# Kernel tuning notes

Measured on AMD Instinct MI355X. Metric: run time of the kernel, lower is better.

## Reference

```python
import jax, jax.numpy as jnp
import numpy as np
jax.config.update("jax_enable_x64", True)

B_GROWTH = 1.38
PS = np.array([1, 19349663, 83492791, 73856093], dtype=np.int64)
N_POINTS = 131072

def _isprime(n):
    if n < 2:
        return False
    i = 2
    while i * i <= n:
        if n % i == 0:
            return False
        i += 1
    return True

def _build_tables():
    n_levels, n_entrys, base_res, f = 16, 2 ** 19, 16, 2
    while not _isprime(n_entrys):
        n_entrys += 1
    xyz_min = np.array([-1.0, -1.0, -1.0])
    xyz_max = np.array([1.0, 1.0, 1.0])
    start_frame, end_frame, total_frame = 0, 99, 100
    bounds = np.stack([
        np.concatenate([xyz_min, [start_frame / total_frame]]),
        np.concatenate([xyz_max, [end_frame / total_frame]]),
    ]).astype(np.float32)
    sizes, nums = [], []
    for i in range(n_levels):
        grid_num = int((base_res * B_GROWTH ** i) ** 3)
        grid_size = ((xyz_max - xyz_min).prod() / grid_num) ** (1.0 / 3.0)
        world_size = (xyz_max - xyz_min) / grid_size
        nums.append(np.concatenate([world_size, [end_frame - start_frame + 1]]).astype(np.int64))
        xyz_size = (xyz_max - xyz_min) / (world_size - 1)
        sizes.append(np.concatenate([xyz_size, [1.0 / (total_frame - 1)]]))
    entrys_size = np.array(sizes, dtype=np.float32)
    entrys_num = np.array(nums, dtype=np.int64)
    start_hash = n_levels
    for i in range(n_levels):
        if int(entrys_num[i].prod()) > n_entrys:
            start_hash = i
            break
    return n_levels, n_entrys, f, bounds, entrys_size, entrys_num, start_hash, start_frame, total_frame

# 16 binary corner offsets, last coord = LSB (matches hard-coded torch table)
OFFSETS = np.array([[(i >> 3) & 1, (i >> 2) & 1, (i >> 1) & 1, i & 1] for i in range(16)], dtype=np.float32)

def setup_inputs() -> dict:
    L, T, f, bounds, entrys_size, entrys_num, start_hash, start_frame, total_frame = _build_tables()
    key = jax.random.key(0)
    k1, k2, k3 = jax.random.split(key, 3)
    xyz = jax.random.uniform(k1, (N_POINTS, 3), dtype=jnp.float32)  # inside [-1,1]^3 bbox
    t = jax.random.uniform(k2, (N_POINTS, 1), dtype=jnp.float32)
    # kaiming_normal_ on (L,T,f): fan_in = T*f, gain=sqrt(2)
    std = float(np.sqrt(2.0 / (T * f)))
    data = jax.random.normal(k3, (L, T, f), dtype=jnp.float32) * std
    return {
        "xyz": xyz, "t": t, "data": data,
        "bounds": jnp.asarray(bounds), "offsets": jnp.asarray(OFFSETS),
        "entrys_size": jnp.asarray(entrys_size), "entrys_num": jnp.asarray(entrys_num),
        "start_hash": int(start_hash), "start_frame": int(start_frame), "total_frame": int(total_frame),
    }

def reference(xyz, t, data, bounds, offsets, entrys_size, entrys_num, start_hash, start_frame, total_frame):
    L, T, f = data.shape
    N = xyz.shape[0]
    t = t - start_frame / (total_frame - 1)
    xyzt = jnp.concatenate([xyz, t], axis=-1)                                   # [N,4]
    float_xyzt = (xyzt[None] - bounds[0][None, None]) / entrys_size[:, None, :]  # [L,N,4]
    int_xyzt = (float_xyzt[:, :, None] + offsets[None, None]).astype(jnp.int64)  # [L,N,16,4]
    offset_xyzt = float_xyzt - int_xyzt[:, :, 0]                                 # [L,N,4]
    int_xyzt = jnp.clip(int_xyzt, 0, (entrys_num - 1)[:, None, None, :])
    en = entrys_num  # int64 [L,4]
    ind_direct = ((int_xyzt[..., 0] * en[:, None, None, 1] + int_xyzt[..., 1]) * en[:, None, None, 2]
                  + int_xyzt[..., 2]) * en[:, None, None, 3] + int_xyzt[..., 3]  # [L,N,16]
    ps = jnp.asarray(PS)
    ind_hash = (int_xyzt[..., 0] * ps[0] ^ int_xyzt[..., 1] * ps[1]
                ^ int_xyzt[..., 2] * ps[2] ^ int_xyzt[..., 3] * ps[3]) % T
    is_hash = (jnp.arange(L) >= start_hash)[:, None, None]
    ind = jnp.where(is_hash, ind_hash, ind_direct)                               # [L,N,16]
    val = jnp.take_along_axis(data, ind.reshape(L, -1, 1), axis=1).reshape(L, N, 16, f)
    w = jnp.clip(1.0 - offsets[None, None] + (2.0 * offsets[None, None] - 1.0) * offset_xyzt[:, :, None], 0.0, 1.0)
    w = jnp.prod(w, axis=-1)                                                     # [L,N,16]
    out = (w[..., None] * val).sum(axis=-2)                                      # [L,N,f]
    return out.transpose(1, 0, 2).reshape(N, L * f)
```

## Files before the change

kernel.cpp:

```cpp
#include <hip/hip_runtime.h>


#define FDIM 2

using f32x2 = __attribute__((ext_vector_type(2))) float;

__global__ __launch_bounds__(256) void mh4d_kernel(
    const float* __restrict__ xyz,
    const float* __restrict__ tt,
    const float* __restrict__ data,
    const float* __restrict__ bounds,
    const float* __restrict__ es,
    const int*   __restrict__ en,
    const int*   __restrict__ p_sh,
    const int*   __restrict__ p_sf,
    const int*   __restrict__ p_tf,
    float* __restrict__ out,
    int N, int L, unsigned int T, unsigned long long M,
    unsigned int bpl)
{
    int l, chunk;
    if ((L & 7) == 0) {
        const unsigned int x   = blockIdx.x & 7u;
        const unsigned int rem = blockIdx.x >> 3;
        const unsigned int p   = rem / bpl;
        chunk = (int)(rem - p * bpl);
        l     = (int)(p * 8u + x);
    } else {
        l     = (int)(blockIdx.x / bpl);
        chunk = (int)(blockIdx.x - (unsigned)l * bpl);
    }
    const int n = chunk * (int)blockDim.x + (int)threadIdx.x;
    if (n >= N) return;

    const int start_hash = *p_sh;
    const float tshift = (float)((double)(*p_sf) / (double)(*p_tf - 1));

    const float es0 = es[l * 4 + 0], es1 = es[l * 4 + 1];
    const float es2 = es[l * 4 + 2], es3 = es[l * 4 + 3];
    const int e0 = en[l * 4 + 0], e1 = en[l * 4 + 1];
    const int e2 = en[l * 4 + 2], e3 = en[l * 4 + 3];

    const float b0 = bounds[0], b1 = bounds[1], b2 = bounds[2], b3 = bounds[3];

    const float x  = __builtin_nontemporal_load(&xyz[n * 3 + 0]);
    const float y  = __builtin_nontemporal_load(&xyz[n * 3 + 1]);
    const float z  = __builtin_nontemporal_load(&xyz[n * 3 + 2]);
    const float tv = __builtin_nontemporal_load(&tt[n]) - tshift;

    const float f0 = (x  - b0) / es0;
    const float f1 = (y  - b1) / es1;
    const float f2 = (z  - b2) / es2;
    const float f3 = (tv - b3) / es3;

    int lo0 = (int)f0, hi0 = (int)(f0 + 1.0f);
    int lo1 = (int)f1, hi1 = (int)(f1 + 1.0f);
    int lo2 = (int)f2, hi2 = (int)(f2 + 1.0f);
    int lo3 = (int)f3, hi3 = (int)(f3 + 1.0f);

    const float o0 = f0 - (float)lo0;
    const float o1 = f1 - (float)lo1;
    const float o2 = f2 - (float)lo2;
    const float o3 = f3 - (float)lo3;

    lo0 = min(max(lo0, 0), e0 - 1);  hi0 = min(max(hi0, 0), e0 - 1);
    lo1 = min(max(lo1, 0), e1 - 1);  hi1 = min(max(hi1, 0), e1 - 1);
    lo2 = min(max(lo2, 0), e2 - 1);  hi2 = min(max(hi2, 0), e2 - 1);
    lo3 = min(max(lo3, 0), e3 - 1);  hi3 = min(max(hi3, 0), e3 - 1);

    unsigned int r16[16];
    if (l >= start_hash) {
        const unsigned long long hx[2] = { (unsigned long long)(unsigned)lo0,
                                           (unsigned long long)(unsigned)hi0 };
        const unsigned long long hy[2] = { (unsigned long long)(unsigned)lo1 * 19349663ull,
                                           (unsigned long long)(unsigned)hi1 * 19349663ull };
        const unsigned long long hz[2] = { (unsigned long long)(unsigned)lo2 * 83492791ull,
                                           (unsigned long long)(unsigned)hi2 * 83492791ull };
        const unsigned long long ht[2] = { (unsigned long long)(unsigned)lo3 * 73856093ull,
                                           (unsigned long long)(unsigned)hi3 * 73856093ull };
        #pragma unroll
        for (int c = 0; c < 16; ++c) {
            const unsigned long long v =
                hx[(c >> 3) & 1] ^ hy[(c >> 2) & 1] ^ hz[(c >> 1) & 1] ^ ht[c & 1];
            const unsigned long long q = __umul64hi(v, M);
            unsigned int r = (unsigned int)v - (unsigned int)q * T;
            if (r >= T) r -= T;
            r16[c] = r;
        }
    } else {
        #pragma unroll
        for (int c = 0; c < 16; ++c) {
            const unsigned int ix = (unsigned)((c & 8) ? hi0 : lo0);
            const unsigned int iy = (unsigned)((c & 4) ? hi1 : lo1);
            const unsigned int iz = (unsigned)((c & 2) ? hi2 : lo2);
            const unsigned int it = (unsigned)((c & 1) ? hi3 : lo3);
            unsigned int ind = ix * (unsigned)e1 + iy;
            ind = ind * (unsigned)e2 + iz;
            ind = ind * (unsigned)e3 + it;
            r16[c] = ind;
        }
    }

    const float* __restrict__ base = data + (size_t)l * (size_t)T * FDIM;
    f32x2 vals[16];
    #pragma unroll
    for (int c = 0; c < 16; ++c) {
        asm volatile("global_load_dwordx2 %0, %1, %2 sc0"
                     : "=v"(vals[c])
                     : "v"(r16[c] * 8u), "s"(base));
    }

    const float wx[2] = { fminf(fmaxf(1.0f - o0, 0.0f), 1.0f), fminf(fmaxf(o0, 0.0f), 1.0f) };
    const float wy[2] = { fminf(fmaxf(1.0f - o1, 0.0f), 1.0f), fminf(fmaxf(o1, 0.0f), 1.0f) };
    const float wz[2] = { fminf(fmaxf(1.0f - o2, 0.0f), 1.0f), fminf(fmaxf(o2, 0.0f), 1.0f) };
    const float wt[2] = { fminf(fmaxf(1.0f - o3, 0.0f), 1.0f), fminf(fmaxf(o3, 0.0f), 1.0f) };

    float pxy[4], pxyz[8], w16[16];
    #pragma unroll
    for (int a = 0; a < 2; ++a)
        #pragma unroll
        for (int b = 0; b < 2; ++b)
            pxy[a * 2 + b] = wx[a] * wy[b];
    #pragma unroll
    for (int a = 0; a < 4; ++a)
        #pragma unroll
        for (int b = 0; b < 2; ++b)
            pxyz[a * 2 + b] = pxy[a] * wz[b];
    #pragma unroll
    for (int a = 0; a < 8; ++a)
        #pragma unroll
        for (int b = 0; b < 2; ++b)
            w16[a * 2 + b] = pxyz[a] * wt[b];

    asm volatile("s_waitcnt vmcnt(0)" ::: "memory");
    __builtin_amdgcn_sched_barrier(0);

    float accx = 0.0f, accy = 0.0f;
    #pragma unroll
    for (int c = 0; c < 16; ++c) {
        accx = fmaf(w16[c], vals[c][0], accx);
        accy = fmaf(w16[c], vals[c][1], accy);
    }

    unsigned long long packed =
        ((unsigned long long)__float_as_uint(accy) << 32) | (unsigned long long)__float_as_uint(accx);
    unsigned long long* op =
        (unsigned long long*)(out + ((size_t)n * (size_t)L + (size_t)l) * FDIM);
    __builtin_nontemporal_store(packed, op);
}

extern "C" void kernel_launch(void* const* d_in, const int* in_sizes, int n_in,
                              void* d_out, int out_size, void* d_ws, size_t ws_size,
                              hipStream_t stream) {
    const float* xyz    = (const float*)d_in[0];
    const float* tt     = (const float*)d_in[1];
    const float* data   = (const float*)d_in[2];
    const float* bounds = (const float*)d_in[3];
    const float* es     = (const float*)d_in[5];
    const int*   en     = (const int*)d_in[6];
    const int*   p_sh   = (const int*)d_in[7];
    const int*   p_sf   = (const int*)d_in[8];
    const int*   p_tf   = (const int*)d_in[9];
    float*       out    = (float*)d_out;

    const int N = in_sizes[0] / 3;
    const int L = in_sizes[5] / 4;
    const unsigned int T = (unsigned int)(in_sizes[2] / (L * FDIM));
    const unsigned long long M = ~0ull / (unsigned long long)T;

    const int threads = 256;
    const unsigned int bpl = (unsigned)((N + threads - 1) / threads);
    dim3 grid(bpl * (unsigned)L);
    mh4d_kernel<<<grid, threads, 0, stream>>>(xyz, tt, data, bounds, es, en,
                                              p_sh, p_sf, p_tf, out,
                                              N, L, T, M, bpl);
}
```

Baseline: 261.4 us.

## Process two points per thread to overlap gathers with weight computation

Each thread now handles two points, issuing 32 gather loads up front and computing weights for the second point while the first point's loads complete. Staged waitcnt values let the first result be accumulated and stored before waiting on the second batch. The grid is halved and launch bounds request 4 blocks per CU. This trades higher register pressure and fewer waves for more memory-level parallelism per wave.

```diff
diff --git a/kernel.cpp b/kernel.cpp
--- a/kernel.cpp
+++ b/kernel.cpp
@@ -5,7 +5,7 @@
 
 using f32x2 = __attribute__((ext_vector_type(2))) float;
 
-__global__ __launch_bounds__(256) void mh4d_kernel(
+__global__ __launch_bounds__(256, 4) void mh4d_kernel(
     const float* __restrict__ xyz,
     const float* __restrict__ tt,
     const float* __restrict__ data,
@@ -21,17 +21,20 @@
 {
     int l, chunk;
     if ((L & 7) == 0) {
-        const unsigned int x   = blockIdx.x & 7u;
+        const unsigned int xb  = blockIdx.x & 7u;
         const unsigned int rem = blockIdx.x >> 3;
         const unsigned int p   = rem / bpl;
         chunk = (int)(rem - p * bpl);
-        l     = (int)(p * 8u + x);
+        l     = (int)(p * 8u + xb);
     } else {
         l     = (int)(blockIdx.x / bpl);
         chunk = (int)(blockIdx.x - (unsigned)l * bpl);
     }
-    const int n = chunk * (int)blockDim.x + (int)threadIdx.x;
-    if (n >= N) return;
+    const int nA = chunk * 2 * (int)blockDim.x + (int)threadIdx.x;
+    if (nA >= N) return;
+    const int nBr = nA + (int)blockDim.x;
+    const bool hasB = nBr < N;
+    const int nB = hasB ? nBr : nA;
 
     const int start_hash = *p_sh;
     const float tshift = (float)((double)(*p_sf) / (double)(*p_tf - 1));
@@ -43,110 +46,143 @@
 
     const float b0 = bounds[0], b1 = bounds[1], b2 = bounds[2], b3 = bounds[3];
 
-    const float x  = __builtin_nontemporal_load(&xyz[n * 3 + 0]);
-    const float y  = __builtin_nontemporal_load(&xyz[n * 3 + 1]);
-    const float z  = __builtin_nontemporal_load(&xyz[n * 3 + 2]);
-    const float tv = __builtin_nontemporal_load(&tt[n]) - tshift;
-
-    const float f0 = (x  - b0) / es0;
-    const float f1 = (y  - b1) / es1;
-    const float f2 = (z  - b2) / es2;
-    const float f3 = (tv - b3) / es3;
-
-    int lo0 = (int)f0, hi0 = (int)(f0 + 1.0f);
-    int lo1 = (int)f1, hi1 = (int)(f1 + 1.0f);
-    int lo2 = (int)f2, hi2 = (int)(f2 + 1.0f);
-    int lo3 = (int)f3, hi3 = (int)(f3 + 1.0f);
-
-    const float o0 = f0 - (float)lo0;
-    const float o1 = f1 - (float)lo1;
-    const float o2 = f2 - (float)lo2;
-    const float o3 = f3 - (float)lo3;
-
-    lo0 = min(max(lo0, 0), e0 - 1);  hi0 = min(max(hi0, 0), e0 - 1);
-    lo1 = min(max(lo1, 0), e1 - 1);  hi1 = min(max(hi1, 0), e1 - 1);
-    lo2 = min(max(lo2, 0), e2 - 1);  hi2 = min(max(hi2, 0), e2 - 1);
-    lo3 = min(max(lo3, 0), e3 - 1);  hi3 = min(max(hi3, 0), e3 - 1);
-
-    unsigned int r16[16];
-    if (l >= start_hash) {
-        const unsigned long long hx[2] = { (unsigned long long)(unsigned)lo0,
-                                           (unsigned long long)(unsigned)hi0 };
-        const unsigned long long hy[2] = { (unsigned long long)(unsigned)lo1 * 19349663ull,
-                                           (unsigned long long)(unsigned)hi1 * 19349663ull };
-        const unsigned long long hz[2] = { (unsigned long long)(unsigned)lo2 * 83492791ull,
-                                           (unsigned long long)(unsigned)hi2 * 83492791ull };
-        const unsigned long long ht[2] = { (unsigned long long)(unsigned)lo3 * 73856093ull,
-                                           (unsigned long long)(unsigned)hi3 * 73856093ull };
-        #pragma unroll
-        for (int c = 0; c < 16; ++c) {
-            const unsigned long long v =
-                hx[(c >> 3) & 1] ^ hy[(c >> 2) & 1] ^ hz[(c >> 1) & 1] ^ ht[c & 1];
-            const unsigned long long q = __umul64hi(v, M);
-            unsigned int r = (unsigned int)v - (unsigned int)q * T;
-            if (r >= T) r -= T;
-            r16[c] = r;
-        }
-    } else {
-        #pragma unroll
-        for (int c = 0; c < 16; ++c) {
-            const unsigned int ix = (unsigned)((c & 8) ? hi0 : lo0);
-            const unsigned int iy = (unsigned)((c & 4) ? hi1 : lo1);
-            const unsigned int iz = (unsigned)((c & 2) ? hi2 : lo2);
-            const unsigned int it = (unsigned)((c & 1) ? hi3 : lo3);
-            unsigned int ind = ix * (unsigned)e1 + iy;
-            ind = ind * (unsigned)e2 + iz;
-            ind = ind * (unsigned)e3 + it;
-            r16[c] = ind;
-        }
+#define LOADP(S, n) \
+    const float x##S  = __builtin_nontemporal_load(&xyz[(n) * 3 + 0]); \
+    const float y##S  = __builtin_nontemporal_load(&xyz[(n) * 3 + 1]); \
+    const float z##S  = __builtin_nontemporal_load(&xyz[(n) * 3 + 2]); \
+    const float tv##S = __builtin_nontemporal_load(&tt[(n)]) - tshift;
+
+    LOADP(A, nA)
+    LOADP(B, nB)
+
+#define CORNERS(S) \
+    const float f0##S = (x##S  - b0) / es0; \
+    const float f1##S = (y##S  - b1) / es1; \
+    const float f2##S = (z##S  - b2) / es2; \
+    const float f3##S = (tv##S - b3) / es3; \
+    int lo0##S = (int)f0##S, hi0##S = (int)(f0##S + 1.0f); \
+    int lo1##S = (int)f1##S, hi1##S = (int)(f1##S + 1.0f); \
+    int lo2##S = (int)f2##S, hi2##S = (int)(f2##S + 1.0f); \
+    int lo3##S = (int)f3##S, hi3##S = (int)(f3##S + 1.0f); \
+    const float o0##S = f0##S - (float)lo0##S; \
+    const float o1##S = f1##S - (float)lo1##S; \
+    const float o2##S = f2##S - (float)lo2##S; \
+    const float o3##S = f3##S - (float)lo3##S; \
+    lo0##S = min(max(lo0##S, 0), e0 - 1);  hi0##S = min(max(hi0##S, 0), e0 - 1); \
+    lo1##S = min(max(lo1##S, 0), e1 - 1);  hi1##S = min(max(hi1##S, 0), e1 - 1); \
+    lo2##S = min(max(lo2##S, 0), e2 - 1);  hi2##S = min(max(hi2##S, 0), e2 - 1); \
+    lo3##S = min(max(lo3##S, 0), e3 - 1);  hi3##S = min(max(hi3##S, 0), e3 - 1);
+
+    CORNERS(A)
+    CORNERS(B)
+
+#define INDICES(S, r) \
+    if (l >= start_hash) { \
+        const unsigned long long hx[2] = { (unsigned long long)(unsigned)lo0##S, \
+                                           (unsigned long long)(unsigned)hi0##S }; \
+        const unsigned long long hy[2] = { (unsigned long long)(unsigned)lo1##S * 19349663ull, \
+                                           (unsigned long long)(unsigned)hi1##S * 19349663ull }; \
+        const unsigned long long hz[2] = { (unsigned long long)(unsigned)lo2##S * 83492791ull, \
+                                           (unsigned long long)(unsigned)hi2##S * 83492791ull }; \
+        const unsigned long long ht[2] = { (unsigned long long)(unsigned)lo3##S * 73856093ull, \
+                                           (unsigned long long)(unsigned)hi3##S * 73856093ull }; \
+        _Pragma("unroll") \
+        for (int c = 0; c < 16; ++c) { \
+            const unsigned long long v = \
+                hx[(c >> 3) & 1] ^ hy[(c >> 2) & 1] ^ hz[(c >> 1) & 1] ^ ht[c & 1]; \
+            const unsigned long long q = __umul64hi(v, M);    \
+            unsigned int rr = (unsigned int)v - (unsigned int)q * T; \
+            if (rr >= T) rr -= T; \
+            (r)[c] = rr; \
+        } \
+    } else { \
+        _Pragma("unroll") \
+        for (int c = 0; c < 16; ++c) { \
+            const unsigned int ix = (unsigned)((c & 8) ? hi0##S : lo0##S); \
+            const unsigned int iy = (unsigned)((c & 4) ? hi1##S : lo1##S); \
+            const unsigned int iz = (unsigned)((c & 2) ? hi2##S : lo2##S); \
+            const unsigned int it = (unsigned)((c & 1) ? hi3##S : lo3##S); \
+            unsigned int ind = ix * (unsigned)e1 + iy; \
+            ind = ind * (unsigned)e2 + iz; \
+            ind = ind * (unsigned)e3 + it; \
+            (r)[c] = ind; \
+        } \
     }
 
     const float* __restrict__ base = data + (size_t)l * (size_t)T * FDIM;
-    f32x2 vals[16];
+
+    __builtin_amdgcn_sched_barrier(0);
+
+    unsigned int rA[16];
+    INDICES(A, rA)
+    f32x2 valsA[16];
+    #pragma unroll
+    for (int c = 0; c < 16; ++c)
+        asm volatile("global_load_dwordx2 %0, %1, %2 sc0"
+                     : "=v"(valsA[c]) : "v"(rA[c] * 8u), "s"(base));
+
+    unsigned int rB[16];
+    INDICES(B, rB)
+    f32x2 valsB[16];
+    #pragma unroll
+    for (int c = 0; c < 16; ++c)
+        asm volatile("global_load_dwordx2 %0, %1, %2 sc0"
+                     : "=v"(valsB[c]) : "v"(rB[c] * 8u), "s"(base));
+
+#define WEIGHTS(S, w) \
+    { \
+        const float wx[2] = { fminf(fmaxf(1.0f - o0##S, 0.0f), 1.0f), fminf(fmaxf(o0##S, 0.0f), 1.0f) }; \
+        const float wy[2] = { fminf(fmaxf(1.0f - o1##S, 0.0f), 1.0f), fminf(fmaxf(o1##S, 0.0f), 1.0f) }; \
+        const float wz[2] = { fminf(fmaxf(1.0f - o2##S, 0.0f), 1.0f), fminf(fmaxf(o2##S, 0.0f), 1.0f) }; \
+        const float wt[2] = { fminf(fmaxf(1.0f - o3##S, 0.0f), 1.0f), fminf(fmaxf(o3##S, 0.0f), 1.0f) }; \
+        float pxy[4], pxyz[8]; \
+        _Pragma("unroll") for (int a = 0; a < 2; ++a) \
+            _Pragma("unroll") for (int b = 0; b < 2; ++b) pxy[a * 2 + b] = wx[a] * wy[b]; \
+        _Pragma("unroll") for (int a = 0; a < 4; ++a) \
+            _Pragma("unroll") for (int b = 0; b < 2; ++b) pxyz[a * 2 + b] = pxy[a] * wz[b]; \
+        _Pragma("unroll") for (int a = 0; a < 8; ++a) \
+            _Pragma("unroll") for (int b = 0; b < 2; ++b) (w)[a * 2 + b] = pxyz[a] * wt[b]; \
+    }
+
+    float wA[16];
+    WEIGHTS(A, wA)
+
+    asm volatile("s_waitcnt vmcnt(16)" ::: "memory");
+    __builtin_amdgcn_sched_barrier(0);
+
+    float accxA = 0.0f, accyA = 0.0f;
     #pragma unroll
     for (int c = 0; c < 16; ++c) {
-        asm volatile("global_load_dwordx2 %0, %1, %2 sc0"
-                     : "=v"(vals[c])
-                     : "v"(r16[c] * 8u), "s"(base));
-    }
-
-    const float wx[2] = { fminf(fmaxf(1.0f - o0, 0.0f), 1.0f), fminf(fmaxf(o0, 0.0f), 1.0f) };
-    const float wy[2] = { fminf(fmaxf(1.0f - o1, 0.0f), 1.0f), fminf(fmaxf(o1, 0.0f), 1.0f) };
-    const float wz[2] = { fminf(fmaxf(1.0f - o2, 0.0f), 1.0f), fminf(fmaxf(o2, 0.0f), 1.0f) };
-    const float wt[2] = { fminf(fmaxf(1.0f - o3, 0.0f), 1.0f), fminf(fmaxf(o3, 0.0f), 1.0f) };
-
-    float pxy[4], pxyz[8], w16[16];
-    #pragma unroll
-    for (int a = 0; a < 2; ++a)
-        #pragma unroll
-        for (int b = 0; b < 2; ++b)
-            pxy[a * 2 + b] = wx[a] * wy[b];
-    #pragma unroll
-    for (int a = 0; a < 4; ++a)
-        #pragma unroll
-        for (int b = 0; b < 2; ++b)
-            pxyz[a * 2 + b] = pxy[a] * wz[b];
-    #pragma unroll
-    for (int a = 0; a < 8; ++a)
-        #pragma unroll
-        for (int b = 0; b < 2; ++b)
-            w16[a * 2 + b] = pxyz[a] * wt[b];
-
-    asm volatile("s_waitcnt vmcnt(0)" ::: "memory");
+        accxA = fmaf(wA[c], valsA[c][0], accxA);
+        accyA = fmaf(wA[c], valsA[c][1], accyA);
+    }
+    {
+        unsigned long long packed =
+            ((unsigned long long)__float_as_uint(accyA) << 32) | (unsigned long long)__float_as_uint(accxA);
+        unsigned long long* op =
+            (unsigned long long*)(out + ((size_t)nA * (size_t)L + (size_t)l) * FDIM);
+        __builtin_nontemporal_store(packed, op);
+    }
+
+    float wB[16];
+    WEIGHTS(B, wB)
+
+    asm volatile("s_waitcnt vmcnt(1)" ::: "memory");
     __builtin_amdgcn_sched_barrier(0);
 
-    float accx = 0.0f, accy = 0.0f;
+    float accxB = 0.0f, accyB = 0.0f;
     #pragma unroll
     for (int c = 0; c < 16; ++c) {
-        accx = fmaf(w16[c], vals[c][0], accx);
-        accy = fmaf(w16[c], vals[c][1], accy);
-    }
-
-    unsigned long long packed =
-        ((unsigned long long)__float_as_uint(accy) << 32) | (unsigned long long)__float_as_uint(accx);
-    unsigned long long* op =
-        (unsigned long long*)(out + ((size_t)n * (size_t)L + (size_t)l) * FDIM);
-    __builtin_nontemporal_store(packed, op);
+        accxB = fmaf(wB[c], valsB[c][0], accxB);
+        accyB = fmaf(wB[c], valsB[c][1], accyB);
+    }
+    if (hasB) {
+        unsigned long long packed =
+            ((unsigned long long)__float_as_uint(accyB) << 32) | (unsigned long long)__float_as_uint(accxB);
+        unsigned long long* op =
+            (unsigned long long*)(out + ((size_t)nB * (size_t)L + (size_t)l) * FDIM);
+        __builtin_nontemporal_store(packed, op);
+    }
 }
 
 extern "C" void kernel_launch(void* const* d_in, const int* in_sizes, int n_in,
@@ -169,7 +205,8 @@
     const unsigned long long M = ~0ull / (unsigned long long)T;
 
     const int threads = 256;
-    const unsigned int bpl = (unsigned)((N + threads - 1) / threads);
+    const int ppb = 2 * threads;
+    const unsigned int bpl = (unsigned)((N + ppb - 1) / ppb);
     dim3 grid(bpl * (unsigned)L);
     mh4d_kernel<<<grid, threads, 0, stream>>>(xyz, tt, data, bounds, es, en,
                                               p_sh, p_sf, p_tf, out,
```

After: 269.3 us. 1.03x slower.
